# Performance work log

Measured on AMD Instinct MI355X. Metric: run time of the kernel, lower is better.

The kernel has to match this reference:

```python
import jax, jax.numpy as jnp
import numpy as np
from jax import lax

C = 64      # mid_channels
CR = 16     # reduced channels (C // reduction_ratio 4)
G = 4       # groups (C // group_channels 16)
K = 7       # involution kernel size
L = 6       # number of involution layers (n_layers - 2)
EPS = 1e-5
DN = ('NCHW', 'OIHW', 'NCHW')


def conv3(x, w, b):
    # 3x3 conv, stride 1, no padding (torch Conv2d default)
    y = lax.conv_general_dilated(x, w, (1, 1), [(0, 0), (0, 0)], dimension_numbers=DN)
    return y + b[None, :, None, None]


def conv1x1(x, w, b):
    # pointwise conv as einsum over channels
    return jnp.einsum('oi,bihw->bohw', w, x) + b[None, :, None, None]


def involution(x, wr, br, g, bt, mu, var, ws, bs):
    B, Cc, H, W = x.shape
    # kernel generation: 1x1 reduce -> BN (eval) -> ReLU -> 1x1 span
    t = conv1x1(x, wr, br)
    t = (t - mu[None, :, None, None]) * (g * jax.lax.rsqrt(var + EPS))[None, :, None, None] + bt[None, :, None, None]
    t = jax.nn.relu(t)
    w = conv1x1(t, ws, bs)                    # (B, G*K*K, H, W)
    w = w.reshape(B, G, K * K, H, W)
    # unfold: patches ordered (C, Kh, Kw) along channel dim, matching torch unfold
    p = lax.conv_general_dilated_patches(x, (K, K), (1, 1), [(K // 2, K // 2)] * 2, dimension_numbers=DN)
    p = p.reshape(B, G, Cc // G, K * K, H, W)
    out = jnp.einsum('bgkhw,bgckhw->bgchw', w, p)
    return out.reshape(B, Cc, H, W)


def setup_inputs() -> dict:
    key = jax.random.key(0)
    ks = jax.random.split(key, 9)
    s = 0.05
    return {
        'input_tensor': jax.random.normal(ks[0], (1, 3, 128, 128), jnp.float32),
        'conv_in_w': jax.random.normal(ks[1], (C, 3, 3, 3), jnp.float32) * s,
        'conv_in_b': jax.random.normal(ks[2], (C,), jnp.float32) * s,
        'w_reduce': jax.random.normal(ks[3], (L, CR, C), jnp.float32) * s,
        'b_reduce': jax.random.normal(ks[4], (L, CR), jnp.float32) * s,
        'bn_gamma': jnp.ones((L, CR), jnp.float32),
        'bn_beta': jnp.zeros((L, CR), jnp.float32),
        'bn_mean': jnp.zeros((L, CR), jnp.float32),
        'bn_var': jnp.ones((L, CR), jnp.float32),
        'w_span': jax.random.normal(ks[5], (L, G * K * K, CR), jnp.float32) * s,
        'b_span': jax.random.normal(ks[6], (L, G * K * K), jnp.float32) * s,
        'conv_out_w': jax.random.normal(ks[7], (2 * C, C, 3, 3), jnp.float32) * s,
        'conv_out_b': jax.random.normal(ks[8], (2 * C,), jnp.float32) * s,
    }


def reference(input_tensor, conv_in_w, conv_in_b, w_reduce, b_reduce, bn_gamma,
              bn_beta, bn_mean, bn_var, w_span, b_span, conv_out_w, conv_out_b):
    x = conv3(input_tensor, conv_in_w, conv_in_b)          # (1, 64, 126, 126)
    for i in range(L):
        x = jax.nn.relu(involution(x, w_reduce[i], b_reduce[i], bn_gamma[i],
                                   bn_beta[i], bn_mean[i], bn_var[i],
                                   w_span[i], b_span[i]))
    return conv3(x, conv_out_w, conv_out_b)                # (1, 128, 124, 124)
```

## Files before the change

### kernel.cpp

```cpp
#include <hip/hip_runtime.h>

#define IH 126
#define IW 126
#define HW 15876
#define OH 124
#define OW 124
#define OHW 15376

__global__ __launch_bounds__(256) void conv_in_kernel(
    const float* __restrict__ x, const float* __restrict__ w,
    const float* __restrict__ b, float* __restrict__ y)
{
  int pix = blockIdx.x * 256 + threadIdx.x;
  if (pix >= HW) return;
  int oc = blockIdx.y;
  int h  = pix / IW;
  int wc = pix - h * IW;
  const float* wp = w + oc * 27;
  float acc = b[oc];
#pragma unroll
  for (int ci = 0; ci < 3; ci++)
#pragma unroll
    for (int ky = 0; ky < 3; ky++)
#pragma unroll
      for (int kx = 0; kx < 3; kx++)
        acc = fmaf(x[ci * 128 * 128 + (h + ky) * 128 + (wc + kx)],
                   wp[ci * 9 + ky * 3 + kx], acc);
  y[oc * HW + pix] = acc;
}

__global__ __launch_bounds__(512, 4) void inv_kernel(
    const float* __restrict__ x, float* __restrict__ y,
    const float* __restrict__ wr, const float* __restrict__ br,
    const float* __restrict__ gam, const float* __restrict__ bet,
    const float* __restrict__ mu, const float* __restrict__ var,
    const float* __restrict__ wspan, const float* __restrict__ bspan)
{
  __shared__ __align__(16) float xs[140][68];
  __shared__ __align__(16) float wvs[6272];
  float* tss = &wvs[5632];
  float* ob  = &xs[0][0];

  int tid = threadIdx.x;
  int bx = blockIdx.x & 15, by = blockIdx.x >> 4;
  int ox0 = bx * 8, oy0 = by * 4;
  int xh0 = ox0 - 3, yh0 = oy0 - 3;

  for (int idx = tid; idx < 140 * 64; idx += 512) {
    int c = idx / 140;
    int pos = idx - c * 140;
    int row = pos / 14;
    int col = pos - row * 14;
    int gy = yh0 + row, gx = xh0 + col;
    float v = 0.f;
    if (gy >= 0 && gy < IH && gx >= 0 && gx < IW)
      v = x[c * HW + gy * IW + gx];
    xs[pos][c] = v;
  }
  __syncthreads();

  int w_ = __builtin_amdgcn_readfirstlane(tid >> 6);
  int ln = tid & 63;
  int p  = ln & 31;
  int prow = p >> 3, pcol = p & 7;
  int pc = (prow + 3) * 14 + (pcol + 3);

  {
    int cr0 = 2 * w_;
    const float* wa = wr + cr0 * 64;
    const float* wb = wa + 64;
    float a0 = 0.f, a1 = 0.f;
#pragma unroll
    for (int ci = 0; ci < 64; ci += 4) {
      float4 xv = *(const float4*)&xs[pc][ci];
      a0 = fmaf(xv.x, wa[ci + 0], a0); a1 = fmaf(xv.x, wb[ci + 0], a1);
      a0 = fmaf(xv.y, wa[ci + 1], a0); a1 = fmaf(xv.y, wb[ci + 1], a1);
      a0 = fmaf(xv.z, wa[ci + 2], a0); a1 = fmaf(xv.z, wb[ci + 2], a1);
      a0 = fmaf(xv.w, wa[ci + 3], a0); a1 = fmaf(xv.w, wb[ci + 3], a1);
    }
    float s0 = gam[cr0]     * rsqrtf(var[cr0]     + 1e-5f);
    float s1 = gam[cr0 + 1] * rsqrtf(var[cr0 + 1] + 1e-5f);
    float t0 = (a0 + br[cr0]     - mu[cr0])     * s0 + bet[cr0];
    float t1 = (a1 + br[cr0 + 1] - mu[cr0 + 1]) * s1 + bet[cr0 + 1];
    if (ln < 32) {
      tss[p * 20 + cr0]     = fmaxf(t0, 0.f);
      tss[p * 20 + cr0 + 1] = fmaxf(t1, 0.f);
    }
  }
  __syncthreads();

  {
    float tv[16];
#pragma unroll
    for (int i = 0; i < 4; i++) {
      float4 t4 = *(const float4*)&tss[p * 20 + 4 * i];
      tv[4 * i] = t4.x; tv[4 * i + 1] = t4.y;
      tv[4 * i + 2] = t4.z; tv[4 * i + 3] = t4.w;
    }
    __syncthreads();
    for (int j = 0; j < 25; j++) {
      int pair = w_ + 8 * j;
      if (pair < 196) {
        const float* wk = wspan + pair * 16;
        float a = bspan[pair];
#pragma unroll
        for (int i = 0; i < 16; i++) a = fmaf(tv[i], wk[i], a);
        if (ln < 32) wvs[pair * 32 + pcol * 4 + prow] = a;
      }
    }
  }
  __syncthreads();

  float acc0 = 0.f, acc1 = 0.f, acc2 = 0.f, acc3 = 0.f;
  {
    int c = ln;
    int g = ln >> 4;
    float xw[4][7];
#pragma unroll
    for (int r = 0; r < 4; r++)
#pragma unroll
      for (int kx = 0; kx < 7; kx++)
        xw[r][kx] = xs[r * 14 + w_ + kx][c];
#pragma unroll
    for (int ky = 0; ky < 7; ky++) {
      if (ky > 0) {
#pragma unroll
        for (int r = 0; r < 3; r++)
#pragma unroll
          for (int kx = 0; kx < 7; kx++) xw[r][kx] = xw[r + 1][kx];
#pragma unroll
        for (int kx = 0; kx < 7; kx++)
          xw[3][kx] = xs[(ky + 3) * 14 + w_ + kx][c];
      }
#pragma unroll
      for (int kx = 0; kx < 7; kx++) {
        int k = ky * 7 + kx;
        float4 w4 = *(const float4*)&wvs[(g * 49 + k) * 32 + w_ * 4];
        acc0 = fmaf(w4.x, xw[0][kx], acc0);
        acc1 = fmaf(w4.y, xw[1][kx], acc1);
        acc2 = fmaf(w4.z, xw[2][kx], acc2);
        acc3 = fmaf(w4.w, xw[3][kx], acc3);
      }
    }
  }
  __syncthreads();

  {
    int c = ln;
    ob[c * 33 + 0 * 8 + w_] = fmaxf(acc0, 0.f);
    ob[c * 33 + 1 * 8 + w_] = fmaxf(acc1, 0.f);
    ob[c * 33 + 2 * 8 + w_] = fmaxf(acc2, 0.f);
    ob[c * 33 + 3 * 8 + w_] = fmaxf(acc3, 0.f);
  }
  __syncthreads();
  for (int j = tid; j < 2048; j += 512) {
    int c2 = j >> 5, pp = j & 31;
    int pr = pp >> 3, pc2 = pp & 7;
    int gy = oy0 + pr, gx = ox0 + pc2;
    if (gy < IH && gx < IW)
      y[c2 * HW + gy * IW + gx] = ob[c2 * 33 + pp];
  }
}

__global__ __launch_bounds__(256) void transpose_w_kernel(
    const float* __restrict__ w, float* __restrict__ wt)
{
  int i = blockIdx.x * 256 + threadIdx.x;
  if (i >= 128 * 64 * 9) return;
  int oc = i / 576;
  int rem = i - oc * 576;
  int ci = rem / 9;
  int k = rem - ci * 9;
  wt[(k * 64 + ci) * 128 + oc] = w[i];
}

__global__ __launch_bounds__(256, 6) void conv_out_kernel(
    const float* __restrict__ x, const float* __restrict__ wt,
    const float* __restrict__ b, float* __restrict__ y)
{
  __shared__ __align__(16) float xsm[16 * 100 * 4];
  int tid = threadIdx.x;
  int bx = blockIdx.x & 15, by = blockIdx.x >> 4;
  int oy0 = by * 8, ox0 = bx * 8;

  for (int u = tid; u < 1600; u += 256) {
    int cq = u / 100;
    int pos = u - cq * 100;
    int row = pos / 10;
    int col = pos - row * 10;
    int gy = oy0 + row, gx = ox0 + col;
    float4 v = make_float4(0.f, 0.f, 0.f, 0.f);
    if (gy < IH && gx < IW) {
      const float* xp = x + cq * 4 * HW + gy * IW + gx;
      v.x = xp[0]; v.y = xp[HW]; v.z = xp[2 * HW]; v.w = xp[3 * HW];
    }
    *(float4*)&xsm[u * 4] = v;
  }
  __syncthreads();

  int ln = tid & 63;
  int px = ln & 7, py = ln >> 3;
  int wv_ = __builtin_amdgcn_readfirstlane(tid >> 6);
  int oc8 = blockIdx.y * 32 + wv_ * 8;

  float acc[8];
#pragma unroll
  for (int j = 0; j < 8; j++) acc[j] = b[oc8 + j];

#pragma unroll
  for (int ky = 0; ky < 3; ky++) {
#pragma unroll
    for (int kx = 0; kx < 3; kx++) {
      int k = ky * 3 + kx;
      int pidx = (py + ky) * 10 + px + kx;
      const float* wp = wt + k * 64 * 128 + oc8;
#pragma unroll 4
      for (int cq = 0; cq < 16; cq++) {
        float4 xv = *(const float4*)&xsm[(cq * 100 + pidx) * 4];
        const float* wq = wp + cq * 4 * 128;
#pragma unroll
        for (int j = 0; j < 8; j++) {
          acc[j] = fmaf(xv.x, wq[0 * 128 + j], acc[j]);
          acc[j] = fmaf(xv.y, wq[1 * 128 + j], acc[j]);
          acc[j] = fmaf(xv.z, wq[2 * 128 + j], acc[j]);
          acc[j] = fmaf(xv.w, wq[3 * 128 + j], acc[j]);
        }
      }
    }
  }

  int oy = oy0 + py, ox = ox0 + px;
  if (oy < OH && ox < OW) {
#pragma unroll
    for (int j = 0; j < 8; j++)
      y[(oc8 + j) * OHW + oy * OW + ox] = acc[j];
  }
}

extern "C" void kernel_launch(void* const* d_in, const int* in_sizes, int n_in,
                              void* d_out, int out_size, void* d_ws, size_t ws_size,
                              hipStream_t stream)
{
  const float* input = (const float*)d_in[0];
  const float* ciw   = (const float*)d_in[1];
  const float* cib   = (const float*)d_in[2];
  const float* wred  = (const float*)d_in[3];
  const float* bred  = (const float*)d_in[4];
  const float* gam   = (const float*)d_in[5];
  const float* bet   = (const float*)d_in[6];
  const float* mu    = (const float*)d_in[7];
  const float* var   = (const float*)d_in[8];
  const float* wspan = (const float*)d_in[9];
  const float* bspan = (const float*)d_in[10];
  const float* cow   = (const float*)d_in[11];
  const float* cob   = (const float*)d_in[12];
  float* out = (float*)d_out;

  float* bufA = (float*)d_ws;
  float* bufB = bufA + (1 << 20);
  float* wt   = bufA + (1 << 21);

  transpose_w_kernel<<<288, 256, 0, stream>>>(cow, wt);
  conv_in_kernel<<<dim3(63, 64), 256, 0, stream>>>(input, ciw, cib, bufA);

  float* cur = bufA; float* nxt = bufB;
  for (int i = 0; i < 6; i++) {
    inv_kernel<<<512, 512, 0, stream>>>(cur, nxt,
        wred + i * 16 * 64, bred + i * 16, gam + i * 16, bet + i * 16,
        mu + i * 16, var + i * 16, wspan + i * 196 * 16, bspan + i * 196);
    float* t = cur; cur = nxt; nxt = t;
  }
  conv_out_kernel<<<dim3(256, 4), 256, 0, stream>>>(cur, wt, cob, out);
}
```

Before: 253.2 us.

## Rewrite output conv as direct register-tiled loads and unroll span-weight generation

The final 3x3 conv no longer stages inputs in LDS. Each thread reads its input rows straight from global memory as float2 vectors and computes 4 adjacent output pixels for 2 output channels. The weights are re-transposed so each wave gets its per-channel weights through uniform loads, and outputs are written as float4. In the involution kernel, the span bias is cached in LDS and the 196-row span loop is fully unrolled with a separate tail, which removes the per-iteration bounds check. The trade-off is that the conv now depends on L1/L2 caching for input reuse across channels instead of explicit shared memory, and it does fewer FMAs per load.

```diff
diff --git a/kernel.cpp b/kernel.cpp
--- a/kernel.cpp
+++ b/kernel.cpp
@@ -38,6 +38,7 @@
 {
   __shared__ __align__(16) float xs[140][68];
   __shared__ __align__(16) float wvs[6272];
+  __shared__ float bsp_l[196];
   float* tss = &wvs[5632];
   float* ob  = &xs[0][0];
 
@@ -46,6 +47,7 @@
   int ox0 = bx * 8, oy0 = by * 4;
   int xh0 = ox0 - 3, yh0 = oy0 - 3;
 
+  if (tid < 196) bsp_l[tid] = bspan[tid];
   for (int idx = tid; idx < 140 * 64; idx += 512) {
     int c = idx / 140;
     int pos = idx - c * 140;
@@ -98,15 +100,22 @@
       tv[4 * i + 2] = t4.z; tv[4 * i + 3] = t4.w;
     }
     __syncthreads();
-    for (int j = 0; j < 25; j++) {
+#pragma unroll
+    for (int j = 0; j < 24; j++) {
       int pair = w_ + 8 * j;
-      if (pair < 196) {
-        const float* wk = wspan + pair * 16;
-        float a = bspan[pair];
-#pragma unroll
-        for (int i = 0; i < 16; i++) a = fmaf(tv[i], wk[i], a);
-        if (ln < 32) wvs[pair * 32 + pcol * 4 + prow] = a;
-      }
+      const float* wk = wspan + pair * 16;
+      float a = bsp_l[pair];
+#pragma unroll
+      for (int i = 0; i < 16; i++) a = fmaf(tv[i], wk[i], a);
+      if (ln < 32) wvs[pair * 32 + pcol * 4 + prow] = a;
+    }
+    if (w_ < 4) {
+      int pair = w_ + 192;
+      const float* wk = wspan + pair * 16;
+      float a = bsp_l[pair];
+#pragma unroll
+      for (int i = 0; i < 16; i++) a = fmaf(tv[i], wk[i], a);
+      if (ln < 32) wvs[pair * 32 + pcol * 4 + prow] = a;
     }
   }
   __syncthreads();
@@ -163,7 +172,7 @@
 }
 
 __global__ __launch_bounds__(256) void transpose_w_kernel(
-    const float* __restrict__ w, float* __restrict__ wt)
+    const float* __restrict__ w, float* __restrict__ wt2)
 {
   int i = blockIdx.x * 256 + threadIdx.x;
   if (i >= 128 * 64 * 9) return;
@@ -171,69 +180,64 @@
   int rem = i - oc * 576;
   int ci = rem / 9;
   int k = rem - ci * 9;
-  wt[(k * 64 + ci) * 128 + oc] = w[i];
-}
-
-__global__ __launch_bounds__(256, 6) void conv_out_kernel(
-    const float* __restrict__ x, const float* __restrict__ wt,
+  int ky = k / 3, kx = k - ky * 3;
+  wt2[(oc >> 1) * 1152 + ky * 384 + ci * 6 + kx * 2 + (oc & 1)] = w[i];
+}
+
+__global__ __launch_bounds__(256) void conv_out_kernel(
+    const float* __restrict__ x, const float* __restrict__ wt2,
     const float* __restrict__ b, float* __restrict__ y)
 {
-  __shared__ __align__(16) float xsm[16 * 100 * 4];
   int tid = threadIdx.x;
-  int bx = blockIdx.x & 15, by = blockIdx.x >> 4;
-  int oy0 = by * 8, ox0 = bx * 8;
-
-  for (int u = tid; u < 1600; u += 256) {
-    int cq = u / 100;
-    int pos = u - cq * 100;
-    int row = pos / 10;
-    int col = pos - row * 10;
-    int gy = oy0 + row, gx = ox0 + col;
-    float4 v = make_float4(0.f, 0.f, 0.f, 0.f);
-    if (gy < IH && gx < IW) {
-      const float* xp = x + cq * 4 * HW + gy * IW + gx;
-      v.x = xp[0]; v.y = xp[HW]; v.z = xp[2 * HW]; v.w = xp[3 * HW];
-    }
-    *(float4*)&xsm[u * 4] = v;
-  }
-  __syncthreads();
-
+  int wv_ = __builtin_amdgcn_readfirstlane(tid >> 6);
   int ln = tid & 63;
-  int px = ln & 7, py = ln >> 3;
-  int wv_ = __builtin_amdgcn_readfirstlane(tid >> 6);
-  int oc8 = blockIdx.y * 32 + wv_ * 8;
-
-  float acc[8];
-#pragma unroll
-  for (int j = 0; j < 8; j++) acc[j] = b[oc8 + j];
-
-#pragma unroll
+  int tx = blockIdx.x & 7, ty = blockIdx.x >> 3;
+  int oc0 = blockIdx.y * 8 + wv_ * 2;
+
+  int row  = ty * 16 + (ln >> 2);
+  int col0 = tx * 16 + (ln & 3) * 4;
+  bool valid = (row < OH) && (col0 < OW);
+  int r0 = valid ? row : 0;
+  int c0 = valid ? col0 : 0;
+
+  const float* wb = wt2 + oc0 * 576;
+  float acc0[4], acc1[4];
+  float bb0 = b[oc0], bb1 = b[oc0 + 1];
+#pragma unroll
+  for (int i = 0; i < 4; i++) { acc0[i] = bb0; acc1[i] = bb1; }
+
   for (int ky = 0; ky < 3; ky++) {
-#pragma unroll
-    for (int kx = 0; kx < 3; kx++) {
-      int k = ky * 3 + kx;
-      int pidx = (py + ky) * 10 + px + kx;
-      const float* wp = wt + k * 64 * 128 + oc8;
-#pragma unroll 4
-      for (int cq = 0; cq < 16; cq++) {
-        float4 xv = *(const float4*)&xsm[(cq * 100 + pidx) * 4];
-        const float* wq = wp + cq * 4 * 128;
-#pragma unroll
-        for (int j = 0; j < 8; j++) {
-          acc[j] = fmaf(xv.x, wq[0 * 128 + j], acc[j]);
-          acc[j] = fmaf(xv.y, wq[1 * 128 + j], acc[j]);
-          acc[j] = fmaf(xv.z, wq[2 * 128 + j], acc[j]);
-          acc[j] = fmaf(xv.w, wq[3 * 128 + j], acc[j]);
-        }
+    const float* xr = x + (r0 + ky) * IW + c0;
+    const float* wk = wb + ky * 384;
+#pragma unroll 8
+    for (int ci = 0; ci < 64; ci++) {
+      const float* xp = xr + ci * HW;
+      float2 u0 = *(const float2*)(xp);
+      float2 u1 = *(const float2*)(xp + 2);
+      float2 u2 = *(const float2*)(xp + 4);
+      float xv[6] = {u0.x, u0.y, u1.x, u1.y, u2.x, u2.y};
+      const float* wc = wk + ci * 6;
+      float w00 = wc[0], w01 = wc[1];
+      float w10 = wc[2], w11 = wc[3];
+      float w20 = wc[4], w21 = wc[5];
+#pragma unroll
+      for (int px = 0; px < 4; px++) {
+        float xa = xv[px], xb = xv[px + 1], xc = xv[px + 2];
+        acc0[px] = fmaf(xa, w00, acc0[px]);
+        acc1[px] = fmaf(xa, w01, acc1[px]);
+        acc0[px] = fmaf(xb, w10, acc0[px]);
+        acc1[px] = fmaf(xb, w11, acc1[px]);
+        acc0[px] = fmaf(xc, w20, acc0[px]);
+        acc1[px] = fmaf(xc, w21, acc1[px]);
       }
     }
   }
 
-  int oy = oy0 + py, ox = ox0 + px;
-  if (oy < OH && ox < OW) {
-#pragma unroll
-    for (int j = 0; j < 8; j++)
-      y[(oc8 + j) * OHW + oy * OW + ox] = acc[j];
+  if (valid) {
+    float4 s0 = make_float4(acc0[0], acc0[1], acc0[2], acc0[3]);
+    float4 s1 = make_float4(acc1[0], acc1[1], acc1[2], acc1[3]);
+    *(float4*)&y[oc0 * OHW + row * OW + col0] = s0;
+    *(float4*)&y[(oc0 + 1) * OHW + row * OW + col0] = s1;
   }
 }
 
@@ -270,5 +274,5 @@
         mu + i * 16, var + i * 16, wspan + i * 196 * 16, bspan + i * 196);
     float* t = cur; cur = nxt; nxt = t;
   }
-  conv_out_kernel<<<dim3(256, 4), 256, 0, stream>>>(cur, wt, cob, out);
-}
+  conv_out_kernel<<<dim3(64, 16), 256, 0, stream>>>(cur, wt, cob, out);
+}
```

Measured after the change: 299.7 us. 1.18x slower.

## Switch intermediate activations to channels-last layout across all kernels

Applied to the files above, without the earlier changes.

Changes the activation buffers from CHW to HWC so each involution block loads a 64-channel pixel with one coalesced wavefront read and writes results directly without a shared-memory transpose stage. conv_in now computes all 64 output channels per thread, holding weights in LDS and writing float4 channel vectors, and is launched with far fewer blocks. The involution kernel pads the xs and wvs LDS arrays to reduce bank conflicts, caches bspan in LDS and unrolls the span loop. Risks include lower parallelism in conv_in (only 63 blocks) and the removed occupancy hint on conv_out.

```diff
diff --git a/kernel.cpp b/kernel.cpp
--- a/kernel.cpp
+++ b/kernel.cpp
@@ -7,60 +7,83 @@
 #define OW 124
 #define OHW 15376
 
+
 __global__ __launch_bounds__(256) void conv_in_kernel(
     const float* __restrict__ x, const float* __restrict__ w,
-    const float* __restrict__ b, float* __restrict__ y)
-{
-  int pix = blockIdx.x * 256 + threadIdx.x;
+    const float* __restrict__ b, float* __restrict__ yt)
+{
+  __shared__ float wl[64 * 28];
+  __shared__ float bl[64];
+  int tid = threadIdx.x;
+  for (int i = tid; i < 1728; i += 256) {
+    int oc = i / 27, r = i - oc * 27;
+    wl[oc * 28 + r] = w[i];
+  }
+  if (tid < 64) bl[tid] = b[tid];
+  __syncthreads();
+
+  int pix = blockIdx.x * 256 + tid;
   if (pix >= HW) return;
-  int oc = blockIdx.y;
-  int h  = pix / IW;
+  int h = pix / IW;
   int wc = pix - h * IW;
-  const float* wp = w + oc * 27;
-  float acc = b[oc];
+  float xr[27];
 #pragma unroll
   for (int ci = 0; ci < 3; ci++)
 #pragma unroll
     for (int ky = 0; ky < 3; ky++)
 #pragma unroll
       for (int kx = 0; kx < 3; kx++)
-        acc = fmaf(x[ci * 128 * 128 + (h + ky) * 128 + (wc + kx)],
-                   wp[ci * 9 + ky * 3 + kx], acc);
-  y[oc * HW + pix] = acc;
+        xr[ci * 9 + ky * 3 + kx] = x[ci * 128 * 128 + (h + ky) * 128 + (wc + kx)];
+
+  float* yp = yt + pix * 64;
+#pragma unroll 1
+  for (int oc4 = 0; oc4 < 64; oc4 += 4) {
+    float4 o;
+    float* op = (float*)&o;
+#pragma unroll
+    for (int j = 0; j < 4; j++) {
+      const float* wp = &wl[(oc4 + j) * 28];
+      float a = bl[oc4 + j];
+#pragma unroll
+      for (int i = 0; i < 27; i++) a = fmaf(xr[i], wp[i], a);
+      op[j] = a;
+    }
+    *(float4*)(yp + oc4) = o;
+  }
 }
 
 __global__ __launch_bounds__(512, 4) void inv_kernel(
-    const float* __restrict__ x, float* __restrict__ y,
+    const float* __restrict__ xt, float* __restrict__ yt,
     const float* __restrict__ wr, const float* __restrict__ br,
     const float* __restrict__ gam, const float* __restrict__ bet,
     const float* __restrict__ mu, const float* __restrict__ var,
     const float* __restrict__ wspan, const float* __restrict__ bspan)
 {
-  __shared__ __align__(16) float xs[140][68];
-  __shared__ __align__(16) float wvs[6272];
-  float* tss = &wvs[5632];
-  float* ob  = &xs[0][0];
+  __shared__ __align__(16) float xs[140 * 65];
+  __shared__ __align__(16) float wvs[6296];
+  __shared__ float bsp_l[196];
+  float* tss = &wvs[5656];
 
   int tid = threadIdx.x;
   int bx = blockIdx.x & 15, by = blockIdx.x >> 4;
   int ox0 = bx * 8, oy0 = by * 4;
   int xh0 = ox0 - 3, yh0 = oy0 - 3;
 
-  for (int idx = tid; idx < 140 * 64; idx += 512) {
-    int c = idx / 140;
-    int pos = idx - c * 140;
-    int row = pos / 14;
-    int col = pos - row * 14;
-    int gy = yh0 + row, gx = xh0 + col;
+  int w_ = __builtin_amdgcn_readfirstlane(tid >> 6);
+  int ln = tid & 63;
+
+  if (tid < 196) bsp_l[tid] = bspan[tid];
+  for (int pos = w_; pos < 140; pos += 8) {
+    int r = pos / 14;
+    int cc = pos - r * 14;
+    int gy = yh0 + r, gx = xh0 + cc;
     float v = 0.f;
     if (gy >= 0 && gy < IH && gx >= 0 && gx < IW)
-      v = x[c * HW + gy * IW + gx];
-    xs[pos][c] = v;
-  }
-  __syncthreads();
-
-  int w_ = __builtin_amdgcn_readfirstlane(tid >> 6);
-  int ln = tid & 63;
+      v = xt[(gy * IW + gx) * 64 + ln];
+    xs[pos * 65 + ln] = v;
+  }
+  __syncthreads();
+
   int p  = ln & 31;
   int prow = p >> 3, pcol = p & 7;
   int pc = (prow + 3) * 14 + (pcol + 3);
@@ -71,12 +94,10 @@
     const float* wb = wa + 64;
     float a0 = 0.f, a1 = 0.f;
 #pragma unroll
-    for (int ci = 0; ci < 64; ci += 4) {
-      float4 xv = *(const float4*)&xs[pc][ci];
-      a0 = fmaf(xv.x, wa[ci + 0], a0); a1 = fmaf(xv.x, wb[ci + 0], a1);
-      a0 = fmaf(xv.y, wa[ci + 1], a0); a1 = fmaf(xv.y, wb[ci + 1], a1);
-      a0 = fmaf(xv.z, wa[ci + 2], a0); a1 = fmaf(xv.z, wb[ci + 2], a1);
-      a0 = fmaf(xv.w, wa[ci + 3], a0); a1 = fmaf(xv.w, wb[ci + 3], a1);
+    for (int ci = 0; ci < 64; ci++) {
+      float xv = xs[pc * 65 + ci];
+      a0 = fmaf(xv, wa[ci], a0);
+      a1 = fmaf(xv, wb[ci], a1);
     }
     float s0 = gam[cr0]     * rsqrtf(var[cr0]     + 1e-5f);
     float s1 = gam[cr0 + 1] * rsqrtf(var[cr0 + 1] + 1e-5f);
@@ -98,29 +119,36 @@
       tv[4 * i + 2] = t4.z; tv[4 * i + 3] = t4.w;
     }
     __syncthreads();
-    for (int j = 0; j < 25; j++) {
+#pragma unroll
+    for (int j = 0; j < 24; j++) {
       int pair = w_ + 8 * j;
-      if (pair < 196) {
-        const float* wk = wspan + pair * 16;
-        float a = bspan[pair];
-#pragma unroll
-        for (int i = 0; i < 16; i++) a = fmaf(tv[i], wk[i], a);
-        if (ln < 32) wvs[pair * 32 + pcol * 4 + prow] = a;
-      }
+      int gc = (pair * 669) >> 15;
+      const float* wk = wspan + pair * 16;
+      float a = bsp_l[pair];
+#pragma unroll
+      for (int i = 0; i < 16; i++) a = fmaf(tv[i], wk[i], a);
+      if (ln < 32) wvs[pair * 32 + gc * 8 + pcol * 4 + prow] = a;
+    }
+    if (w_ < 4) {
+      int pair = w_ + 192;
+      const float* wk = wspan + pair * 16;
+      float a = bsp_l[pair];
+#pragma unroll
+      for (int i = 0; i < 16; i++) a = fmaf(tv[i], wk[i], a);
+      if (ln < 32) wvs[pair * 32 + 24 + pcol * 4 + prow] = a;
     }
   }
   __syncthreads();
 
   float acc0 = 0.f, acc1 = 0.f, acc2 = 0.f, acc3 = 0.f;
   {
-    int c = ln;
-    int g = ln >> 4;
+    int gb = (ln >> 4) * 1576;
     float xw[4][7];
 #pragma unroll
     for (int r = 0; r < 4; r++)
 #pragma unroll
       for (int kx = 0; kx < 7; kx++)
-        xw[r][kx] = xs[r * 14 + w_ + kx][c];
+        xw[r][kx] = xs[(r * 14 + w_ + kx) * 65 + ln];
 #pragma unroll
     for (int ky = 0; ky < 7; ky++) {
       if (ky > 0) {
@@ -130,12 +158,12 @@
           for (int kx = 0; kx < 7; kx++) xw[r][kx] = xw[r + 1][kx];
 #pragma unroll
         for (int kx = 0; kx < 7; kx++)
-          xw[3][kx] = xs[(ky + 3) * 14 + w_ + kx][c];
+          xw[3][kx] = xs[((ky + 3) * 14 + w_ + kx) * 65 + ln];
       }
 #pragma unroll
       for (int kx = 0; kx < 7; kx++) {
         int k = ky * 7 + kx;
-        float4 w4 = *(const float4*)&wvs[(g * 49 + k) * 32 + w_ * 4];
+        float4 w4 = *(const float4*)&wvs[gb + k * 32 + w_ * 4];
         acc0 = fmaf(w4.x, xw[0][kx], acc0);
         acc1 = fmaf(w4.y, xw[1][kx], acc1);
         acc2 = fmaf(w4.z, xw[2][kx], acc2);
@@ -143,22 +171,15 @@
       }
     }
   }
-  __syncthreads();
-
-  {
-    int c = ln;
-    ob[c * 33 + 0 * 8 + w_] = fmaxf(acc0, 0.f);
-    ob[c * 33 + 1 * 8 + w_] = fmaxf(acc1, 0.f);
-    ob[c * 33 + 2 * 8 + w_] = fmaxf(acc2, 0.f);
-    ob[c * 33 + 3 * 8 + w_] = fmaxf(acc3, 0.f);
-  }
-  __syncthreads();
-  for (int j = tid; j < 2048; j += 512) {
-    int c2 = j >> 5, pp = j & 31;
-    int pr = pp >> 3, pc2 = pp & 7;
-    int gy = oy0 + pr, gx = ox0 + pc2;
-    if (gy < IH && gx < IW)
-      y[c2 * HW + gy * IW + gx] = ob[c2 * 33 + pp];
+
+  {
+    int gx = ox0 + w_;
+    if (gx < IW) {
+      if (oy0 + 0 < IH) yt[((oy0 + 0) * IW + gx) * 64 + ln] = fmaxf(acc0, 0.f);
+      if (oy0 + 1 < IH) yt[((oy0 + 1) * IW + gx) * 64 + ln] = fmaxf(acc1, 0.f);
+      if (oy0 + 2 < IH) yt[((oy0 + 2) * IW + gx) * 64 + ln] = fmaxf(acc2, 0.f);
+      if (oy0 + 3 < IH) yt[((oy0 + 3) * IW + gx) * 64 + ln] = fmaxf(acc3, 0.f);
+    }
   }
 }
 
@@ -174,8 +195,8 @@
   wt[(k * 64 + ci) * 128 + oc] = w[i];
 }
 
-__global__ __launch_bounds__(256, 6) void conv_out_kernel(
-    const float* __restrict__ x, const float* __restrict__ wt,
+__global__ __launch_bounds__(256) void conv_out_kernel(
+    const float* __restrict__ xt, const float* __restrict__ wt,
     const float* __restrict__ b, float* __restrict__ y)
 {
   __shared__ __align__(16) float xsm[16 * 100 * 4];
@@ -190,10 +211,8 @@
     int col = pos - row * 10;
     int gy = oy0 + row, gx = ox0 + col;
     float4 v = make_float4(0.f, 0.f, 0.f, 0.f);
-    if (gy < IH && gx < IW) {
-      const float* xp = x + cq * 4 * HW + gy * IW + gx;
-      v.x = xp[0]; v.y = xp[HW]; v.z = xp[2 * HW]; v.w = xp[3 * HW];
-    }
+    if (gy < IH && gx < IW)
+      v = *(const float4*)&xt[(gy * IW + gx) * 64 + cq * 4];
     *(float4*)&xsm[u * 4] = v;
   }
   __syncthreads();
@@ -261,7 +280,7 @@
   float* wt   = bufA + (1 << 21);
 
   transpose_w_kernel<<<288, 256, 0, stream>>>(cow, wt);
-  conv_in_kernel<<<dim3(63, 64), 256, 0, stream>>>(input, ciw, cib, bufA);
+  conv_in_kernel<<<63, 256, 0, stream>>>(input, ciw, cib, bufA);
 
   float* cur = bufA; float* nxt = bufB;
   for (int i = 0; i < 6; i++) {
```

Result: slower. 989.9 us (+290.9%).
